# Kernel tuning notes

Measured on AMD Instinct MI355X. Metric: run time of the kernel, lower is better.

## Reference

```python
import jax, jax.numpy as jnp
import numpy as np

N = 50000      # nodes
E = 1600000    # edges (avg degree 32)
C_IN = 128
C_H = 128
C_OUT = 10
G = 512        # number of graphs in the batch


def setup_inputs() -> dict:
    key = jax.random.key(0)
    ks = jax.random.split(key, 16)
    x = jax.random.normal(ks[0], (N, C_IN), dtype=jnp.float32)
    edge_index = jax.random.randint(ks[1], (2, E), 0, N, dtype=jnp.int64)
    batch = jnp.sort(jax.random.randint(ks[2], (N,), 0, G, dtype=jnp.int64))

    def lin(k, fan_in, fan_out):
        lim = 1.0 / np.sqrt(fan_in)
        return jax.random.uniform(k, (fan_in, fan_out), jnp.float32, -lim, lim)

    return {
        "x": x, "edge_index": edge_index, "batch": batch,
        # conv1: c_in -> c_hidden
        "Wr1": lin(ks[3], C_IN, C_H), "br1": jnp.zeros((C_H,), jnp.float32),
        "Wo1": lin(ks[4], C_IN, C_H),
        # conv2: c_hidden -> 2*c_hidden
        "Wr2": lin(ks[5], C_H, 2 * C_H), "br2": jnp.zeros((2 * C_H,), jnp.float32),
        "Wo2": lin(ks[6], C_H, 2 * C_H),
        # conv3: 2*c_hidden -> c_hidden
        "Wr3": lin(ks[7], 2 * C_H, C_H), "br3": jnp.zeros((C_H,), jnp.float32),
        "Wo3": lin(ks[8], 2 * C_H, C_H),
        # head
        "W1": lin(ks[9], C_H, 4 * C_OUT), "b1": jnp.zeros((4 * C_OUT,), jnp.float32),
        "W2": lin(ks[10], 4 * C_OUT, C_OUT), "b2": jnp.zeros((C_OUT,), jnp.float32),
    }


def _graph_conv(x, src, dst, Wr, br, Wo):
    # PyG GraphConv: lin_rel(sum_{j in N(i)} x_j) + lin_root(x_i)
    agg = jax.ops.segment_sum(x[src], dst, num_segments=N)  # [N, F_in]
    return agg @ Wr + br + x @ Wo


def reference(x, edge_index, batch, Wr1, br1, Wo1, Wr2, br2, Wo2,
              Wr3, br3, Wo3, W1, b1, W2, b2):
    src, dst = edge_index[0], edge_index[1]
    h = jax.nn.relu(_graph_conv(x, src, dst, Wr1, br1, Wo1))
    h = jax.nn.relu(_graph_conv(h, src, dst, Wr2, br2, Wo2))
    h = _graph_conv(h, src, dst, Wr3, br3, Wo3)
    # global mean pool over graphs
    sums = jax.ops.segment_sum(h, batch, num_segments=G)            # [G, C_H]
    cnts = jax.ops.segment_sum(jnp.ones((N,), h.dtype), batch, num_segments=G)
    pooled = sums / jnp.maximum(cnts, 1.0)[:, None]
    # dropout is identity in eval mode
    out = pooled @ W1 + b1
    out = out @ W2 + b2
    return out
```

## Files before the change

### kernel.cpp

```cpp
#include <hip/hip_runtime.h>
#include <hip/hip_bf16.h>
#include <cstddef>

#define NN 50000
#define EE 1600000
#define GG 512
#define NB 196
#define BSTRIDE 16384
#define BCAP 10240
#define XBLKS 6250
#define SCBLKS 782

typedef unsigned int u32;
typedef unsigned short u16;
typedef __attribute__((ext_vector_type(8))) short frag_ab;
typedef __attribute__((ext_vector_type(4))) float frag_cd;

__device__ __forceinline__ void gl_lds16(const void* g, void* l) {
    __builtin_amdgcn_global_load_lds(
        (const __attribute__((address_space(1))) u32*)g,
        (__attribute__((address_space(3))) u32*)l, 16, 0, 0);
}
__device__ __forceinline__ float b2f_lo(u32 v) { return __uint_as_float(v << 16); }
__device__ __forceinline__ float b2f_hi(u32 v) { return __uint_as_float(v & 0xffff0000u); }
__device__ __forceinline__ float b2f(u32 v, int odd) { return odd ? b2f_hi(v) : b2f_lo(v); }
__device__ __forceinline__ u16 f2b(float x) {
    __hip_bfloat16 h = __float2bfloat16(x);
    return *(u16*)&h;
}
__device__ __forceinline__ u32 pack2(float lo, float hi) {
    return ((u32)f2b(hi) << 16) | f2b(lo);
}
__device__ __forceinline__ void acc2(float2& a, u32 v) {
    a.x += b2f_lo(v);
    a.y += b2f_hi(v);
}



__global__ __launch_bounds__(256) void bscatter_prep_kernel(
    const int* __restrict__ ei, int* __restrict__ bcnt, u32* __restrict__ pairs,
    const float* __restrict__ x, u16* __restrict__ ax,
    const float* __restrict__ Wr1, const float* __restrict__ Wo1,
    const float* __restrict__ Wr2, const float* __restrict__ Wo2,
    const float* __restrict__ Wr3, const float* __restrict__ Wo3,
    const float* __restrict__ br3,
    u16* __restrict__ BT1, u16* __restrict__ BT2, u16* __restrict__ BT3,
    float* __restrict__ bias3) {
    __shared__ int lcnt[NB];
    __shared__ int lbase[NB];
    __shared__ unsigned short lpos[2048];
    int bid = blockIdx.x, t = threadIdx.x;
    if (bid < SCBLKS) {
        int e0 = bid * 2048;
        u32 pk[8];
        int bk[8];
        for (int i = t; i < NB; i += 256) lcnt[i] = 0;
        __syncthreads();
#pragma unroll
        for (int i = 0; i < 8; ++i) {
            int e = e0 + i * 256 + t;
            if (e < EE) {
                int dst = ei[EE + e], src = ei[e];
                int b = dst >> 8;
                bk[i] = b;
                pk[i] = ((u32)src << 8) | (u32)(dst & 255);
                lpos[i * 256 + t] = (unsigned short)atomicAdd(&lcnt[b], 1);
            } else bk[i] = -1;
        }
        __syncthreads();
        for (int i = t; i < NB; i += 256) lbase[i] = atomicAdd(&bcnt[i], lcnt[i]);
        __syncthreads();
#pragma unroll
        for (int i = 0; i < 8; ++i) {
            if (bk[i] >= 0) {
                int pos = lbase[bk[i]] + (int)lpos[i * 256 + t];
                pairs[(size_t)bk[i] * BSTRIDE + pos] = pk[i];
            }
        }
    } else if (bid < SCBLKS + XBLKS) {
        int idx = (bid - SCBLKS) * 256 + t;
        int row = idx >> 5, q = idx & 31;
        float4 v = *(const float4*)(x + (size_t)row * 128 + q * 4);
        *(u32*)(ax + (size_t)row * 256 + 128 + q * 4) = pack2(v.x, v.y);
        *(u32*)(ax + (size_t)row * 256 + 128 + q * 4 + 2) = pack2(v.z, v.w);
    } else {
        int m = bid - SCBLKS - XBLKS;
        int k = t;
        BT2[m * 256 + k] = f2b(k < 128 ? Wr2[k * 256 + m] : Wo2[(k - 128) * 256 + m]);
        BT3[m * 256 + k] = f2b(m < 128 ? Wr3[k * 128 + m] : Wo3[k * 128 + (m - 128)]);
        if (m < 128)
            BT1[m * 256 + k] = f2b(k < 128 ? Wr1[k * 128 + m] : Wo1[(k - 128) * 128 + m]);
        if (k == 0) bias3[m] = (m < 128) ? 0.f : br3[m - 128];
    }
}


__global__ __launch_bounds__(512) void bfill_kernel(const u32* __restrict__ pairs,
                                                    const int* __restrict__ bcnt,
                                                    int* __restrict__ ofs,
                                                    u16* __restrict__ srcl) {
    __shared__ int sc[256];
    __shared__ int cnts[256];
    __shared__ int lcnt[256];
    __shared__ int lcur[256];
    __shared__ int lbuf[BCAP];
    int b = blockIdx.x, t = threadIdx.x;
    if (t < 256) {
        int c = (t < NB) ? bcnt[t] : 0;
        cnts[t] = c;
        sc[t] = c;
        lcnt[t] = 0;
    }
    __syncthreads();
    for (int off = 1; off < 256; off <<= 1) {
        int v = (t >= off && t < 256) ? sc[t - off] : 0;
        __syncthreads();
        if (t < 256) sc[t] += v;
        __syncthreads();
    }
    int base = sc[b] - cnts[b];
    int span = cnts[b];
    const u32* pp = pairs + (size_t)b * BSTRIDE;
    for (int j = t; j < span; j += 512) atomicAdd(&lcnt[pp[j] & 255u], 1);
    __syncthreads();
    int nc = 0;
    if (t < 256) {
        nc = lcnt[t];
        sc[t] = nc;
    }
    __syncthreads();
    for (int off = 1; off < 256; off <<= 1) {
        int v = (t >= off && t < 256) ? sc[t - off] : 0;
        __syncthreads();
        if (t < 256) sc[t] += v;
        __syncthreads();
    }
    if (t < 256) {
        int excl = sc[t] - nc;
        int node = b * 256 + t;
        if (node < NN) ofs[node] = base + excl;
        lcur[t] = excl;
    }
    if (b == 0 && t == 256) ofs[NN] = EE;
    __syncthreads();
    for (int j = t; j < span; j += 512) {
        u32 p = pp[j];
        int pos = atomicAdd(&lcur[p & 255u], 1);
        int src = (int)(p >> 8);
        if (pos < BCAP) lbuf[pos] = src;
        else srcl[base + pos] = (u16)src;
    }
    __syncthreads();
    int lim = span < BCAP ? span : BCAP;
    for (int j = t; j < lim; j += 512) srcl[base + j] = (u16)lbuf[j];
}


__global__ __launch_bounds__(256) void pull_bf_kernel(const u32* __restrict__ Xu,
                                                      const int* __restrict__ ofs,
                                                      const u16* __restrict__ srcl,
                                                      u32* __restrict__ outu) {
    int node = (blockIdx.x * 256 + threadIdx.x) >> 6;
    int lane = threadIdx.x & 63;
    int q = lane >> 4, l = lane & 15;
    int lo = ofs[node], hi = ofs[node + 1];
    float2 a0 = {0.f, 0.f}, a1 = {0.f, 0.f}, a2 = {0.f, 0.f}, a3 = {0.f, 0.f};
    int j = lo;
    for (; j + 15 < hi; j += 16) {
        int s0 = srcl[j + q], s1 = srcl[j + 4 + q];
        int s2 = srcl[j + 8 + q], s3 = srcl[j + 12 + q];
        uint4 v0 = *(const uint4*)(Xu + (size_t)s0 * 128 + l * 4);
        uint4 v1 = *(const uint4*)(Xu + (size_t)s1 * 128 + l * 4);
        uint4 v2 = *(const uint4*)(Xu + (size_t)s2 * 128 + l * 4);
        uint4 v3 = *(const uint4*)(Xu + (size_t)s3 * 128 + l * 4);
        acc2(a0, v0.x); acc2(a1, v0.y); acc2(a2, v0.z); acc2(a3, v0.w);
        acc2(a0, v1.x); acc2(a1, v1.y); acc2(a2, v1.z); acc2(a3, v1.w);
        acc2(a0, v2.x); acc2(a1, v2.y); acc2(a2, v2.z); acc2(a3, v2.w);
        acc2(a0, v3.x); acc2(a1, v3.y); acc2(a2, v3.z); acc2(a3, v3.w);
    }
    for (; j + 3 < hi; j += 4) {
        int s = srcl[j + q];
        uint4 v = *(const uint4*)(Xu + (size_t)s * 128 + l * 4);
        acc2(a0, v.x); acc2(a1, v.y); acc2(a2, v.z); acc2(a3, v.w);
    }
    if (j + q < hi) {
        int s = srcl[j + q];
        uint4 v = *(const uint4*)(Xu + (size_t)s * 128 + l * 4);
        acc2(a0, v.x); acc2(a1, v.y); acc2(a2, v.z); acc2(a3, v.w);
    }
    float acc[8] = {a0.x, a0.y, a1.x, a1.y, a2.x, a2.y, a3.x, a3.y};
#pragma unroll
    for (int i = 0; i < 8; ++i) {
        acc[i] += __shfl_xor(acc[i], 16, 64);
        acc[i] += __shfl_xor(acc[i], 32, 64);
    }
    if (q == 0) {
        uint4 r;
        r.x = pack2(acc[0], acc[1]);
        r.y = pack2(acc[2], acc[3]);
        r.z = pack2(acc[4], acc[5]);
        r.w = pack2(acc[6], acc[7]);
        *(uint4*)(outu + (size_t)node * 128 + l * 4) = r;
    }
}

__global__ __launch_bounds__(256) void pull3_kernel(const u32* __restrict__ Tu,
                                                    const int* __restrict__ ofs,
                                                    const u16* __restrict__ srcl,
                                                    u32* __restrict__ h3u) {
    int node = (blockIdx.x * 256 + threadIdx.x) >> 6;
    int lane = threadIdx.x & 63;
    int q = lane >> 4, l = lane & 15;
    int lo = ofs[node], hi = ofs[node + 1];
    float2 a0 = {0.f, 0.f}, a1 = {0.f, 0.f}, a2 = {0.f, 0.f}, a3 = {0.f, 0.f};
    int j = lo;
    for (; j + 15 < hi; j += 16) {
        int s0 = srcl[j + q], s1 = srcl[j + 4 + q];
        int s2 = srcl[j + 8 + q], s3 = srcl[j + 12 + q];
        uint4 v0 = *(const uint4*)(Tu + (size_t)s0 * 128 + l * 4);
        uint4 v1 = *(const uint4*)(Tu + (size_t)s1 * 128 + l * 4);
        uint4 v2 = *(const uint4*)(Tu + (size_t)s2 * 128 + l * 4);
        uint4 v3 = *(const uint4*)(Tu + (size_t)s3 * 128 + l * 4);
        acc2(a0, v0.x); acc2(a1, v0.y); acc2(a2, v0.z); acc2(a3, v0.w);
        acc2(a0, v1.x); acc2(a1, v1.y); acc2(a2, v1.z); acc2(a3, v1.w);
        acc2(a0, v2.x); acc2(a1, v2.y); acc2(a2, v2.z); acc2(a3, v2.w);
        acc2(a0, v3.x); acc2(a1, v3.y); acc2(a2, v3.z); acc2(a3, v3.w);
    }
    for (; j + 3 < hi; j += 4) {
        int s = srcl[j + q];
        uint4 v = *(const uint4*)(Tu + (size_t)s * 128 + l * 4);
        acc2(a0, v.x); acc2(a1, v.y); acc2(a2, v.z); acc2(a3, v.w);
    }
    if (j + q < hi) {
        int s = srcl[j + q];
        uint4 v = *(const uint4*)(Tu + (size_t)s * 128 + l * 4);
        acc2(a0, v.x); acc2(a1, v.y); acc2(a2, v.z); acc2(a3, v.w);
    }
    float acc[8] = {a0.x, a0.y, a1.x, a1.y, a2.x, a2.y, a3.x, a3.y};
#pragma unroll
    for (int i = 0; i < 8; ++i) {
        acc[i] += __shfl_xor(acc[i], 16, 64);
        acc[i] += __shfl_xor(acc[i], 32, 64);
    }
    if (q == 0) {
        uint4 o = *(const uint4*)(Tu + (size_t)node * 128 + 64 + l * 4);
        acc[0] += b2f_lo(o.x); acc[1] += b2f_hi(o.x);
        acc[2] += b2f_lo(o.y); acc[3] += b2f_hi(o.y);
        acc[4] += b2f_lo(o.z); acc[5] += b2f_hi(o.z);
        acc[6] += b2f_lo(o.w); acc[7] += b2f_hi(o.w);
        uint4 r;
        r.x = pack2(acc[0], acc[1]);
        r.y = pack2(acc[2], acc[3]);
        r.z = pack2(acc[4], acc[5]);
        r.w = pack2(acc[6], acc[7]);
        *(uint4*)(h3u + (size_t)node * 64 + l * 4) = r;
    }
}


__global__ __launch_bounds__(256, 2) void gemm_bf_kernel(
    const u16* __restrict__ A, const u16* __restrict__ BT,
    const float* __restrict__ bias, u16* __restrict__ C,
    int ldc, int coloff, int relu) {
    __shared__ alignas(16) u16 As[128 * 32];
    __shared__ alignas(16) u16 Bs[128 * 32];
    const int t = threadIdx.x;
    const int lane = t & 63, wid = t >> 6;
    const int quad = lane >> 4, l16 = lane & 15;
    const int wm = wid >> 1, wn = wid & 1;
    const int row0 = blockIdx.y * 128, c0 = blockIdx.x * 128;

    frag_cd acc[4][4];
#pragma unroll
    for (int i = 0; i < 4; ++i)
#pragma unroll
        for (int j = 0; j < 4; ++j) acc[i][j] = (frag_cd)0.f;

    const int ca = t, cb = t + 256;
    const int ra = ca >> 2, oa = (ca & 3) * 8;
    const int rb = cb >> 2, ob = (cb & 3) * 8;
    const int garow = min(row0 + ra, NN - 1);
    const int gbrow = min(row0 + rb, NN - 1);
    const size_t gA1 = (size_t)garow * 256 + oa;
    const size_t gA2 = (size_t)gbrow * 256 + ob;
    const size_t gB1 = (size_t)(c0 + ra) * 256 + oa;
    const size_t gB2 = (size_t)(c0 + rb) * 256 + ob;

    for (int kk = 0; kk < 256; kk += 32) {
        __syncthreads();
        gl_lds16(A + gA1 + kk, &As[ca * 8]);
        gl_lds16(A + gA2 + kk, &As[cb * 8]);
        gl_lds16(BT + gB1 + kk, &Bs[ca * 8]);
        gl_lds16(BT + gB2 + kk, &Bs[cb * 8]);
        __syncthreads();

        frag_ab a[4], b[4];
#pragma unroll
        for (int mt = 0; mt < 4; ++mt)
            a[mt] = *(const frag_ab*)&As[(wm * 64 + mt * 16 + l16) * 32 + quad * 8];
#pragma unroll
        for (int nt = 0; nt < 4; ++nt)
            b[nt] = *(const frag_ab*)&Bs[(wn * 64 + nt * 16 + l16) * 32 + quad * 8];
#pragma unroll
        for (int mt = 0; mt < 4; ++mt)
#pragma unroll
            for (int nt = 0; nt < 4; ++nt)
                acc[mt][nt] = __builtin_amdgcn_mfma_f32_16x16x32_bf16(
                    a[mt], b[nt], acc[mt][nt], 0, 0, 0);
    }

#pragma unroll
    for (int nt = 0; nt < 4; ++nt) {
        int col = c0 + wn * 64 + nt * 16 + l16;
        float bv = bias[col];
#pragma unroll
        for (int mt = 0; mt < 4; ++mt) {
#pragma unroll
            for (int r = 0; r < 4; ++r) {
                int row = row0 + wm * 64 + mt * 16 + quad * 4 + r;
                if (row < NN) {
                    float v = acc[mt][nt][r] + bv;
                    if (relu) v = fmaxf(v, 0.f);
                    C[(size_t)row * ldc + coloff + col] = f2b(v);
                }
            }
        }
    }
}


__global__ __launch_bounds__(256, 2) void gemm23_kernel(
    const u16* __restrict__ A, const u16* __restrict__ BT2,
    const float* __restrict__ br2, const u16* __restrict__ BT3,
    const float* __restrict__ bias3, u16* __restrict__ C) {
    __shared__ alignas(16) u16 As[128 * 32];
    __shared__ alignas(16) u16 Bs[128 * 32];
    __shared__ alignas(16) u16 Hs[128 * 256];
    const int t = threadIdx.x;
    const int lane = t & 63, wid = t >> 6;
    const int quad = lane >> 4, l16 = lane & 15;
    const int wm = wid >> 1, wn = wid & 1;
    const int row0 = blockIdx.x * 128;

    const int ca = t, cb = t + 256;
    const int ra = ca >> 2, oa = (ca & 3) * 8;
    const int rb = cb >> 2, ob = (cb & 3) * 8;
    const int garow = min(row0 + ra, NN - 1);
    const int gbrow = min(row0 + rb, NN - 1);
    const size_t gA1 = (size_t)garow * 256 + oa;
    const size_t gA2 = (size_t)gbrow * 256 + ob;

    for (int nb = 0; nb < 2; ++nb) {
        const int c0 = nb * 128;
        frag_cd acc[4][4];
#pragma unroll
        for (int i = 0; i < 4; ++i)
#pragma unroll
            for (int j = 0; j < 4; ++j) acc[i][j] = (frag_cd)0.f;

        for (int kk = 0; kk < 256; kk += 32) {
            __syncthreads();
            gl_lds16(A + gA1 + kk, &As[ca * 8]);
            gl_lds16(A + gA2 + kk, &As[cb * 8]);
            gl_lds16(BT2 + (size_t)(c0 + ra) * 256 + kk + oa, &Bs[ca * 8]);
            gl_lds16(BT2 + (size_t)(c0 + rb) * 256 + kk + ob, &Bs[cb * 8]);
            __syncthreads();

            frag_ab a[4], b[4];
#pragma unroll
            for (int mt = 0; mt < 4; ++mt)
                a[mt] = *(const frag_ab*)&As[(wm * 64 + mt * 16 + l16) * 32 + quad * 8];
#pragma unroll
            for (int nt = 0; nt < 4; ++nt)
                b[nt] = *(const frag_ab*)&Bs[(wn * 64 + nt * 16 + l16) * 32 + quad * 8];
#pragma unroll
            for (int mt = 0; mt < 4; ++mt)
#pragma unroll
                for (int nt = 0; nt < 4; ++nt)
                    acc[mt][nt] = __builtin_amdgcn_mfma_f32_16x16x32_bf16(
                        a[mt], b[nt], acc[mt][nt], 0, 0, 0);
        }
#pragma unroll
        for (int nt = 0; nt < 4; ++nt) {
            int col = c0 + wn * 64 + nt * 16 + l16;
            float bv = br2[col];
#pragma unroll
            for (int mt = 0; mt < 4; ++mt) {
#pragma unroll
                for (int r = 0; r < 4; ++r) {
                    int lr = wm * 64 + mt * 16 + quad * 4 + r;
                    float v = fmaxf(acc[mt][nt][r] + bv, 0.f);
                    Hs[(lr * 256 + col) ^ ((lr & 7) << 3)] = f2b(v);
                }
            }
        }
    }
    __syncthreads();

    for (int nb = 0; nb < 2; ++nb) {
        const int c0 = nb * 128;
        frag_cd acc[4][4];
#pragma unroll
        for (int i = 0; i < 4; ++i)
#pragma unroll
            for (int j = 0; j < 4; ++j) acc[i][j] = (frag_cd)0.f;

        for (int kk = 0; kk < 256; kk += 32) {
            __syncthreads();
            gl_lds16(BT3 + (size_t)(c0 + ra) * 256 + kk + oa, &Bs[ca * 8]);
            gl_lds16(BT3 + (size_t)(c0 + rb) * 256 + kk + ob, &Bs[cb * 8]);
            __syncthreads();

            frag_ab a[4], b[4];
#pragma unroll
            for (int mt = 0; mt < 4; ++mt) {
                int lr = wm * 64 + mt * 16 + l16;
                a[mt] = *(const frag_ab*)&Hs[(lr * 256 + kk + quad * 8) ^ ((lr & 7) << 3)];
            }
#pragma unroll
            for (int nt = 0; nt < 4; ++nt)
                b[nt] = *(const frag_ab*)&Bs[(wn * 64 + nt * 16 + l16) * 32 + quad * 8];
#pragma unroll
            for (int mt = 0; mt < 4; ++mt)
#pragma unroll
                for (int nt = 0; nt < 4; ++nt)
                    acc[mt][nt] = __builtin_amdgcn_mfma_f32_16x16x32_bf16(
                        a[mt], b[nt], acc[mt][nt], 0, 0, 0);
        }
#pragma unroll
        for (int nt = 0; nt < 4; ++nt) {
            int col = c0 + wn * 64 + nt * 16 + l16;
            float bv = bias3[col];
#pragma unroll
            for (int mt = 0; mt < 4; ++mt) {
#pragma unroll
                for (int r = 0; r < 4; ++r) {
                    int row = row0 + wm * 64 + mt * 16 + quad * 4 + r;
                    if (row < NN) {
                        float v = acc[mt][nt][r] + bv;
                        C[(size_t)row * 256 + col] = f2b(v);
                    }
                }
            }
        }
    }
}


__device__ inline int lower_bound_i(const int* a, int n, int v) {
    int lo = 0, hi = n;
    while (lo < hi) {
        int m = (lo + hi) >> 1;
        if (a[m] < v) lo = m + 1; else hi = m;
    }
    return lo;
}

__global__ __launch_bounds__(256) void pool_head_kernel(const u32* __restrict__ h3u,
                                                        const int* __restrict__ batch,
                                                        const float* __restrict__ W1,
                                                        const float* __restrict__ b1,
                                                        const float* __restrict__ W2,
                                                        const float* __restrict__ b2,
                                                        float* __restrict__ out) {
    __shared__ float ps[256];
    __shared__ float p[128];
    __shared__ float hid[40];
    int g = blockIdx.x, t = threadIdx.x;
    int c = t & 127, half = t >> 7;
    int w = c >> 1, odd = c & 1;
    int lo = lower_bound_i(batch, NN, g);
    int hi = lower_bound_i(batch, NN, g + 1);
    float s = 0.f;
    int i = lo + half;
    for (; i + 6 < hi; i += 8) {
        u32 v0 = h3u[(size_t)i * 64 + w];
        u32 v1 = h3u[(size_t)(i + 2) * 64 + w];
        u32 v2 = h3u[(size_t)(i + 4) * 64 + w];
        u32 v3 = h3u[(size_t)(i + 6) * 64 + w];
        s += (b2f(v0, odd) + b2f(v1, odd)) + (b2f(v2, odd) + b2f(v3, odd));
    }
    for (; i < hi; i += 2) s += b2f(h3u[(size_t)i * 64 + w], odd);
    ps[t] = s;
    __syncthreads();
    if (half == 0) p[c] = (ps[c] + ps[c + 128]) / fmaxf((float)(hi - lo), 1.f);
    __syncthreads();
    if (t < 40) {
        float v = b1[t];
        for (int k = 0; k < 128; ++k) v += p[k] * W1[k * 40 + t];
        hid[t] = v;
    }
    __syncthreads();
    if (t < 10) {
        float v = b2[t];
        for (int j = 0; j < 40; ++j) v += hid[j] * W2[j * 10 + t];
        out[g * 10 + t] = v;
    }
}


extern "C" void kernel_launch(void* const* d_in, const int* in_sizes, int n_in,
                              void* d_out, int out_size, void* d_ws, size_t ws_size,
                              hipStream_t stream) {
    const float* x   = (const float*)d_in[0];
    const int* ei    = (const int*)d_in[1];
    const int* batch = (const int*)d_in[2];
    const float* Wr1 = (const float*)d_in[3];
    const float* br1 = (const float*)d_in[4];
    const float* Wo1 = (const float*)d_in[5];
    const float* Wr2 = (const float*)d_in[6];
    const float* br2 = (const float*)d_in[7];
    const float* Wo2 = (const float*)d_in[8];
    const float* Wr3 = (const float*)d_in[9];
    const float* br3 = (const float*)d_in[10];
    const float* Wo3 = (const float*)d_in[11];
    const float* W1  = (const float*)d_in[12];
    const float* b1  = (const float*)d_in[13];
    const float* W2  = (const float*)d_in[14];
    const float* b2  = (const float*)d_in[15];
    float* out = (float*)d_out;

    char* ws = (char*)d_ws;
    size_t off = 0;
    auto alloc = [&](size_t bytes) {
        void* p = ws + off;
        off += (bytes + 255) & ~(size_t)255;
        return p;
    };
    int* ofs      = (int*)alloc((NN + 1) * sizeof(int));
    int* bcnt     = (int*)alloc(256 * sizeof(int));
    u16* srcl     = (u16*)alloc((size_t)EE * 2);
    u16* ax       = (u16*)alloc((size_t)NN * 256 * 2);
    u16* ah1      = (u16*)alloc((size_t)NN * 256 * 2);
    u16* t3o3     = (u16*)alloc((size_t)NN * 256 * 2);
    u16* h3       = (u16*)alloc((size_t)NN * 128 * 2);
    u16* BT1      = (u16*)alloc(128 * 256 * 2);
    u16* BT2      = (u16*)alloc(256 * 256 * 2);
    u16* BT3      = (u16*)alloc(256 * 256 * 2);
    float* bias3  = (float*)alloc(256 * sizeof(float));
    u32* pairs = (u32*)t3o3;

    hipMemsetAsync(bcnt, 0, 256 * sizeof(int), stream);

    bscatter_prep_kernel<<<SCBLKS + XBLKS + 256, 256, 0, stream>>>(
        ei, bcnt, pairs, x, ax, Wr1, Wo1, Wr2, Wo2, Wr3, Wo3, br3,
        BT1, BT2, BT3, bias3);
    bfill_kernel<<<NB, 512, 0, stream>>>(pairs, bcnt, ofs, srcl);

    pull_bf_kernel<<<NN * 64 / 256, 256, 0, stream>>>((const u32*)ax + 64, ofs, srcl, (u32*)ax);
    gemm_bf_kernel<<<dim3(1, 391), 256, 0, stream>>>(ax, BT1, br1, ah1, 256, 128, 1);
    pull_bf_kernel<<<NN * 64 / 256, 256, 0, stream>>>((const u32*)ah1 + 64, ofs, srcl, (u32*)ah1);
    gemm23_kernel<<<391, 256, 0, stream>>>(ah1, BT2, br2, BT3, bias3, t3o3);
    pull3_kernel<<<NN * 64 / 256, 256, 0, stream>>>((const u32*)t3o3, ofs, srcl, (u32*)h3);

    pool_head_kernel<<<GG, 256, 0, stream>>>((const u32*)h3, batch, W1, b1, W2, b2, out);
}
```

Baseline: 352.5 us.

## Fuse final aggregation into per-graph mean pool and head kernel

Removes the separate third pull kernel and the h3 intermediate. Because the third conv is linear and ends in a mean pool, each graph block sums the gathered source rows over all edges whose destination lies in that graph, plus the root term rows, then pools and runs the MLP head. This drops one kernel launch and a full N×128 write and read. In exchange, parallelism falls to 512 blocks of 1024 threads, and the work per block depends on the graph's edge count, which can leave the load unbalanced. It also assumes the CSR edges are sorted by destination and that batch is sorted.

```diff
diff --git a/kernel.cpp b/kernel.cpp
--- a/kernel.cpp
+++ b/kernel.cpp
@@ -205,59 +205,6 @@
     }
 }
 
-__global__ __launch_bounds__(256) void pull3_kernel(const u32* __restrict__ Tu,
-                                                    const int* __restrict__ ofs,
-                                                    const u16* __restrict__ srcl,
-                                                    u32* __restrict__ h3u) {
-    int node = (blockIdx.x * 256 + threadIdx.x) >> 6;
-    int lane = threadIdx.x & 63;
-    int q = lane >> 4, l = lane & 15;
-    int lo = ofs[node], hi = ofs[node + 1];
-    float2 a0 = {0.f, 0.f}, a1 = {0.f, 0.f}, a2 = {0.f, 0.f}, a3 = {0.f, 0.f};
-    int j = lo;
-    for (; j + 15 < hi; j += 16) {
-        int s0 = srcl[j + q], s1 = srcl[j + 4 + q];
-        int s2 = srcl[j + 8 + q], s3 = srcl[j + 12 + q];
-        uint4 v0 = *(const uint4*)(Tu + (size_t)s0 * 128 + l * 4);
-        uint4 v1 = *(const uint4*)(Tu + (size_t)s1 * 128 + l * 4);
-        uint4 v2 = *(const uint4*)(Tu + (size_t)s2 * 128 + l * 4);
-        uint4 v3 = *(const uint4*)(Tu + (size_t)s3 * 128 + l * 4);
-        acc2(a0, v0.x); acc2(a1, v0.y); acc2(a2, v0.z); acc2(a3, v0.w);
-        acc2(a0, v1.x); acc2(a1, v1.y); acc2(a2, v1.z); acc2(a3, v1.w);
-        acc2(a0, v2.x); acc2(a1, v2.y); acc2(a2, v2.z); acc2(a3, v2.w);
-        acc2(a0, v3.x); acc2(a1, v3.y); acc2(a2, v3.z); acc2(a3, v3.w);
-    }
-    for (; j + 3 < hi; j += 4) {
-        int s = srcl[j + q];
-        uint4 v = *(const uint4*)(Tu + (size_t)s * 128 + l * 4);
-        acc2(a0, v.x); acc2(a1, v.y); acc2(a2, v.z); acc2(a3, v.w);
-    }
-    if (j + q < hi) {
-        int s = srcl[j + q];
-        uint4 v = *(const uint4*)(Tu + (size_t)s * 128 + l * 4);
-        acc2(a0, v.x); acc2(a1, v.y); acc2(a2, v.z); acc2(a3, v.w);
-    }
-    float acc[8] = {a0.x, a0.y, a1.x, a1.y, a2.x, a2.y, a3.x, a3.y};
-#pragma unroll
-    for (int i = 0; i < 8; ++i) {
-        acc[i] += __shfl_xor(acc[i], 16, 64);
-        acc[i] += __shfl_xor(acc[i], 32, 64);
-    }
-    if (q == 0) {
-        uint4 o = *(const uint4*)(Tu + (size_t)node * 128 + 64 + l * 4);
-        acc[0] += b2f_lo(o.x); acc[1] += b2f_hi(o.x);
-        acc[2] += b2f_lo(o.y); acc[3] += b2f_hi(o.y);
-        acc[4] += b2f_lo(o.z); acc[5] += b2f_hi(o.z);
-        acc[6] += b2f_lo(o.w); acc[7] += b2f_hi(o.w);
-        uint4 r;
-        r.x = pack2(acc[0], acc[1]);
-        r.y = pack2(acc[2], acc[3]);
-        r.z = pack2(acc[4], acc[5]);
-        r.w = pack2(acc[6], acc[7]);
-        *(uint4*)(h3u + (size_t)node * 64 + l * 4) = r;
-    }
-}
-
 
 __global__ __launch_bounds__(256, 2) void gemm_bf_kernel(
     const u16* __restrict__ A, const u16* __restrict__ BT,
@@ -457,34 +404,96 @@
     return lo;
 }
 
-__global__ __launch_bounds__(256) void pool_head_kernel(const u32* __restrict__ h3u,
-                                                        const int* __restrict__ batch,
-                                                        const float* __restrict__ W1,
-                                                        const float* __restrict__ b1,
-                                                        const float* __restrict__ W2,
-                                                        const float* __restrict__ b2,
-                                                        float* __restrict__ out) {
-    __shared__ float ps[256];
+__global__ __launch_bounds__(1024) void pool3_kernel(
+    const u32* __restrict__ Tu, const int* __restrict__ ofs,
+    const u16* __restrict__ srcl, const int* __restrict__ batch,
+    const float* __restrict__ W1, const float* __restrict__ b1,
+    const float* __restrict__ W2, const float* __restrict__ b2,
+    float* __restrict__ out) {
+    __shared__ float red[16][128];
+    __shared__ float po[8][128];
     __shared__ float p[128];
     __shared__ float hid[40];
     int g = blockIdx.x, t = threadIdx.x;
-    int c = t & 127, half = t >> 7;
-    int w = c >> 1, odd = c & 1;
-    int lo = lower_bound_i(batch, NN, g);
-    int hi = lower_bound_i(batch, NN, g + 1);
-    float s = 0.f;
-    int i = lo + half;
-    for (; i + 6 < hi; i += 8) {
-        u32 v0 = h3u[(size_t)i * 64 + w];
-        u32 v1 = h3u[(size_t)(i + 2) * 64 + w];
-        u32 v2 = h3u[(size_t)(i + 4) * 64 + w];
-        u32 v3 = h3u[(size_t)(i + 6) * 64 + w];
-        s += (b2f(v0, odd) + b2f(v1, odd)) + (b2f(v2, odd) + b2f(v3, odd));
-    }
-    for (; i < hi; i += 2) s += b2f(h3u[(size_t)i * 64 + w], odd);
-    ps[t] = s;
-    __syncthreads();
-    if (half == 0) p[c] = (ps[c] + ps[c + 128]) / fmaxf((float)(hi - lo), 1.f);
+    int w = t >> 6, lane = t & 63;
+    int q = lane >> 4, l = lane & 15;
+    int n_lo = lower_bound_i(batch, NN, g);
+    int n_hi = lower_bound_i(batch, NN, g + 1);
+    int glo = ofs[n_lo], ghi = ofs[n_hi];
+
+    float2 a0 = {0.f, 0.f}, a1 = {0.f, 0.f}, a2 = {0.f, 0.f}, a3 = {0.f, 0.f};
+    for (int gb = glo + w * 64; gb < ghi; gb += 1024) {
+        int nedge = ghi - gb;
+        if (nedge > 64) nedge = 64;
+        int idx = (lane < nedge) ? (int)srcl[gb + lane] : 0;
+        if (nedge == 64) {
+            int s0 = __shfl(idx, q, 64);
+            int s1 = __shfl(idx, 4 + q, 64);
+            int s2 = __shfl(idx, 8 + q, 64);
+            int s3 = __shfl(idx, 12 + q, 64);
+            uint4 v0 = *(const uint4*)(Tu + (size_t)s0 * 128 + l * 4);
+            uint4 v1 = *(const uint4*)(Tu + (size_t)s1 * 128 + l * 4);
+            uint4 v2 = *(const uint4*)(Tu + (size_t)s2 * 128 + l * 4);
+            uint4 v3 = *(const uint4*)(Tu + (size_t)s3 * 128 + l * 4);
+#pragma unroll
+            for (int b = 1; b < 4; ++b) {
+                int u0 = __shfl(idx, b * 16 + q, 64);
+                int u1 = __shfl(idx, b * 16 + 4 + q, 64);
+                int u2 = __shfl(idx, b * 16 + 8 + q, 64);
+                int u3 = __shfl(idx, b * 16 + 12 + q, 64);
+                uint4 w0 = *(const uint4*)(Tu + (size_t)u0 * 128 + l * 4);
+                uint4 w1 = *(const uint4*)(Tu + (size_t)u1 * 128 + l * 4);
+                uint4 w2 = *(const uint4*)(Tu + (size_t)u2 * 128 + l * 4);
+                uint4 w3 = *(const uint4*)(Tu + (size_t)u3 * 128 + l * 4);
+                acc2(a0, v0.x); acc2(a1, v0.y); acc2(a2, v0.z); acc2(a3, v0.w);
+                acc2(a0, v1.x); acc2(a1, v1.y); acc2(a2, v1.z); acc2(a3, v1.w);
+                acc2(a0, v2.x); acc2(a1, v2.y); acc2(a2, v2.z); acc2(a3, v2.w);
+                acc2(a0, v3.x); acc2(a1, v3.y); acc2(a2, v3.z); acc2(a3, v3.w);
+                v0 = w0; v1 = w1; v2 = w2; v3 = w3;
+            }
+            acc2(a0, v0.x); acc2(a1, v0.y); acc2(a2, v0.z); acc2(a3, v0.w);
+            acc2(a0, v1.x); acc2(a1, v1.y); acc2(a2, v1.z); acc2(a3, v1.w);
+            acc2(a0, v2.x); acc2(a1, v2.y); acc2(a2, v2.z); acc2(a3, v2.w);
+            acc2(a0, v3.x); acc2(a1, v3.y); acc2(a2, v3.z); acc2(a3, v3.w);
+        } else {
+#pragma unroll
+            for (int b = 0; b < 4; ++b) {
+#pragma unroll
+                for (int sl = 0; sl < 4; ++sl) {
+                    int e = b * 16 + sl * 4 + q;
+                    int s = __shfl(idx, e, 64);
+                    if (e < nedge) {
+                        uint4 v = *(const uint4*)(Tu + (size_t)s * 128 + l * 4);
+                        acc2(a0, v.x); acc2(a1, v.y); acc2(a2, v.z); acc2(a3, v.w);
+                    }
+                }
+            }
+        }
+    }
+    float acc[8] = {a0.x, a0.y, a1.x, a1.y, a2.x, a2.y, a3.x, a3.y};
+#pragma unroll
+    for (int i = 0; i < 8; ++i) {
+        acc[i] += __shfl_xor(acc[i], 16, 64);
+        acc[i] += __shfl_xor(acc[i], 32, 64);
+    }
+    if (q == 0) {
+#pragma unroll
+        for (int i = 0; i < 8; ++i) red[w][l * 8 + i] = acc[i];
+    }
+    float so = 0.f;
+    int ch = t & 127, rg = t >> 7;
+    for (int r = n_lo + rg; r < n_hi; r += 8)
+        so += b2f(Tu[(size_t)r * 128 + 64 + (ch >> 1)], ch & 1);
+    po[rg][ch] = so;
+    __syncthreads();
+    if (t < 128) {
+        float s = 0.f;
+#pragma unroll
+        for (int k = 0; k < 16; ++k) s += red[k][t];
+#pragma unroll
+        for (int k = 0; k < 8; ++k) s += po[k][t];
+        p[t] = s / fmaxf((float)(n_hi - n_lo), 1.f);
+    }
     __syncthreads();
     if (t < 40) {
         float v = b1[t];
@@ -534,7 +543,6 @@
     u16* ax       = (u16*)alloc((size_t)NN * 256 * 2);
     u16* ah1      = (u16*)alloc((size_t)NN * 256 * 2);
     u16* t3o3     = (u16*)alloc((size_t)NN * 256 * 2);
-    u16* h3       = (u16*)alloc((size_t)NN * 128 * 2);
     u16* BT1      = (u16*)alloc(128 * 256 * 2);
     u16* BT2      = (u16*)alloc(256 * 256 * 2);
     u16* BT3      = (u16*)alloc(256 * 256 * 2);
@@ -552,7 +560,7 @@
     gemm_bf_kernel<<<dim3(1, 391), 256, 0, stream>>>(ax, BT1, br1, ah1, 256, 128, 1);
     pull_bf_kernel<<<NN * 64 / 256, 256, 0, stream>>>((const u32*)ah1 + 64, ofs, srcl, (u32*)ah1);
     gemm23_kernel<<<391, 256, 0, stream>>>(ah1, BT2, br2, BT3, bias3, t3o3);
-    pull3_kernel<<<NN * 64 / 256, 256, 0, stream>>>((const u32*)t3o3, ofs, srcl, (u32*)h3);
-
-    pool_head_kernel<<<GG, 256, 0, stream>>>((const u32*)h3, batch, W1, b1, W2, b2, out);
-}
+
+    pool3_kernel<<<GG, 1024, 0, stream>>>((const u32*)t3o3, ofs, srcl, batch,
+                                          W1, b1, W2, b2, out);
+}
```

New measurement: 352.1 us. About the same (-0.1%).
